# Optimization experiments

Hardware: AMD Instinct MI355X
Metric: run time of the kernel (lower is better)

Reference implementation:

```python
import jax, jax.numpy as jnp
import numpy as np

N_NODES = 4096
N_EDGES = 16384
L = 512
MP_STEPS = 5
DT = 0.01


def _mlp(x, W1, b1, W2, b2):
    return jax.nn.relu(x @ W1 + b1) @ W2 + b2


def _ln(x):
    m = jnp.mean(x, axis=-1, keepdims=True)
    v = jnp.var(x, axis=-1, keepdims=True)
    return (x - m) * jax.lax.rsqrt(v + 1e-6)


_PARAM_SHAPES = [
    ("enc_e_W1", (1, L)), ("enc_e_b1", (L,)), ("enc_e_W2", (L, L)), ("enc_e_b2", (L,)),
    ("enc_n_W1", (1, L)), ("enc_n_b1", (L,)), ("enc_n_W2", (L, L)), ("enc_n_b2", (L,)),
    ("proc_e_W1", (3 * L, L)), ("proc_e_b1", (L,)), ("proc_e_W2", (L, L)), ("proc_e_b2", (L,)),
    ("proc_n_W1", (2 * L, L)), ("proc_n_b1", (L,)), ("proc_n_W2", (L, L)), ("proc_n_b2", (L,)),
    ("dec_e_W1", (L, L)), ("dec_e_b1", (L,)), ("dec_e_W2", (L, 1)), ("dec_e_b2", (1,)),
]


def setup_inputs() -> dict:
    key = jax.random.key(0)
    ks = jax.random.split(key, 3 + len(_PARAM_SHAPES))
    d = {}
    d["state"] = jax.random.normal(ks[0], (N_EDGES + N_NODES,), dtype=jnp.float32)
    d["senders"] = jax.random.randint(ks[1], (N_EDGES,), 0, N_NODES)
    d["receivers"] = jax.random.randint(ks[2], (N_EDGES,), 0, N_NODES)
    for i, (name, shp) in enumerate(_PARAM_SHAPES):
        if name.endswith(("b1", "b2")):
            d[name] = jnp.zeros(shp, dtype=jnp.float32)
        else:
            d[name] = 0.02 * jax.random.normal(ks[3 + i], shp, dtype=jnp.float32)
    return d


def _hamiltonian(x, senders, receivers,
                 enc_e_W1, enc_e_b1, enc_e_W2, enc_e_b2,
                 enc_n_W1, enc_n_b1, enc_n_W2, enc_n_b2,
                 proc_e_W1, proc_e_b1, proc_e_W2, proc_e_b2,
                 proc_n_W1, proc_n_b1, proc_n_W2, proc_n_b2,
                 dec_e_W1, dec_e_b1, dec_e_W2, dec_e_b2):
    # graph_from_state: edge scalars then node scalars
    e = x[:N_EDGES].reshape(N_EDGES, 1)
    n = x[N_EDGES:].reshape(N_NODES, 1)
    # encode (MLP + layer norm)
    eh = _ln(_mlp(e, enc_e_W1, enc_e_b1, enc_e_W2, enc_e_b2))  # [E, L]
    nh = _ln(_mlp(n, enc_n_W1, enc_n_b1, enc_n_W2, enc_n_b2))  # [N, L]
    # process: num_mp_steps of GraphNetwork-style message passing, shared params
    for _ in range(MP_STEPS):
        msg_in = jnp.concatenate([eh, nh[senders], nh[receivers]], axis=-1)  # [E, 3L]
        eh = eh + _mlp(msg_in, proc_e_W1, proc_e_b1, proc_e_W2, proc_e_b2)
        agg = jax.ops.segment_sum(eh, receivers, num_segments=N_NODES)  # [N, L]
        node_in = jnp.concatenate([nh, agg], axis=-1)  # [N, 2L]
        nh = nh + _mlp(node_in, proc_n_W1, proc_n_b1, proc_n_W2, proc_n_b2)
    # decode edges to scalars; H = sum of decoded edge energies
    dec_e = _mlp(eh, dec_e_W1, dec_e_b1, dec_e_W2, dec_e_b2)  # [E, 1]
    return jnp.sum(dec_e)


def reference(state, senders, receivers,
              enc_e_W1, enc_e_b1, enc_e_W2, enc_e_b2,
              enc_n_W1, enc_n_b1, enc_n_W2, enc_n_b2,
              proc_e_W1, proc_e_b1, proc_e_W2, proc_e_b2,
              proc_n_W1, proc_n_b1, proc_n_W2, proc_n_b2,
              dec_e_W1, dec_e_b1, dec_e_W2, dec_e_b2):
    def H_fn(x):
        return _hamiltonian(x, senders, receivers,
                            enc_e_W1, enc_e_b1, enc_e_W2, enc_e_b2,
                            enc_n_W1, enc_n_b1, enc_n_W2, enc_n_b2,
                            proc_e_W1, proc_e_b1, proc_e_W2, proc_e_b2,
                            proc_n_W1, proc_n_b1, proc_n_W2, proc_n_b2,
                            dec_e_W1, dec_e_b1, dec_e_W2, dec_e_b2)
    H, dH = jax.value_and_grad(H_fn)(state)
    # one integrator step driven by the Hamiltonian gradient (stand-in for DAE solve)
    next_state = state - DT * dH
    return next_state
```

## Files before the change

### kernel.cpp

```cpp
#include <hip/hip_runtime.h>


#define E_ROWS 16384
#define N_ROWS 4096
#define DT_F   0.01f

typedef unsigned char u8;
typedef unsigned short u16;
typedef __attribute__((ext_vector_type(8))) short short8v;
typedef __attribute__((ext_vector_type(4))) float f32x4;

__device__ __forceinline__ u16 f2b(float f) {
    union { float f; unsigned u; } v; v.f = f;
    unsigned r = v.u + 0x7FFF + ((v.u >> 16) & 1);
    return (u16)(r >> 16);
}
__device__ __forceinline__ float b2f(u16 u) {
    union { unsigned u; float f; } v; v.u = ((unsigned)u) << 16;
    return v.f;
}

template<int BM, int WM, int WN, int KTOT, int LDA, int LDC,
         bool ADD_C, bool GATHER2, bool BIAS, bool RELU_MASK, bool APPLY_MASK,
         bool WF32, bool WBF16, bool DUALOUT, bool ROWDOT, bool DECW2>
__global__ __launch_bounds__(256)
void bgemm(const u16* __restrict__ A, const u16* __restrict__ Bt,
           float* __restrict__ C, u16* __restrict__ Cb,
           const u16* __restrict__ Cinb, const float* __restrict__ bias,
           const u16* __restrict__ G12b,
           const int* __restrict__ sidx, const int* __restrict__ ridx,
           u8* __restrict__ maskw, u16* __restrict__ C2b,
           const float* __restrict__ wvec, float* __restrict__ outp)
{
    constexpr int BN = WN * 64;
    constexpr int NA = BM / 16;
    constexpr int TC = (BM + BN) / 16;
    constexpr int PER = TC / 4;
    constexpr int IFRAG = BM / WM / 16;
    __shared__ u16 Ls[TC * 512];

    const int tid = threadIdx.x;
    const int lane = tid & 63;
    const int wv = tid >> 6;
    const int wr = wv / WN;
    const int wc = wv % WN;

    const int gx = gridDim.x;
    int id = blockIdx.y * gx + blockIdx.x;
    const int nwg = gx * gridDim.y;
    id = (id & 7) * (nwg >> 3) + (id >> 3);
    const int bx = id % gx;
    const int by = id / gx;
    const int rowBase = by * BM;
    const int colBase = bx * BN;

    const int srow = lane & 15;
    const int slotk = (lane >> 4) << 3;

    const u16* srcs[PER];
    u16* dsts[PER];
#pragma unroll
    for (int q = 0; q < PER; ++q) {
        const int c = wv + (q << 2);
        if (c < NA)
            srcs[q] = A + (size_t)(rowBase + c * 16 + srow) * LDA + slotk;
        else
            srcs[q] = Bt + (size_t)(colBase + (c - NA) * 16 + srow) * KTOT + slotk;
        dsts[q] = Ls + c * 512;
    }

    f32x4 acc[IFRAG][4];
#pragma unroll
    for (int i = 0; i < IFRAG; ++i)
#pragma unroll
        for (int j = 0; j < 4; ++j)
            acc[i][j] = (f32x4){0.f, 0.f, 0.f, 0.f};

    const int fro = ((lane >> 4) << 7) + ((lane & 15) << 3);

    for (int kb = 0; kb < KTOT; kb += 32) {
#pragma unroll
        for (int q = 0; q < PER; ++q)
            __builtin_amdgcn_global_load_lds(
                (const __attribute__((address_space(1))) void*)(srcs[q] + kb),
                (__attribute__((address_space(3))) void*)dsts[q], 16, 0, 0);
        __syncthreads();
        short8v af[IFRAG], bfm[4];
#pragma unroll
        for (int i = 0; i < IFRAG; ++i)
            af[i] = *(const short8v*)&Ls[((wr * IFRAG + i) << 9) + fro];
#pragma unroll
        for (int j = 0; j < 4; ++j)
            bfm[j] = *(const short8v*)&Ls[((NA + (wc << 2) + j) << 9) + fro];
#pragma unroll
        for (int i = 0; i < IFRAG; ++i)
#pragma unroll
            for (int j = 0; j < 4; ++j)
                acc[i][j] = __builtin_amdgcn_mfma_f32_16x16x32_bf16(af[i], bfm[j], acc[i][j], 0, 0, 0);
        __syncthreads();
    }

    const int colB = colBase + wc * 64 + (lane & 15);
    const int rowB = rowBase + wr * (BM / WM) + ((lane >> 4) << 2);
    float bcol[4], wv4[4];
    if (BIAS) {
#pragma unroll
        for (int j = 0; j < 4; ++j) bcol[j] = bias[colB + (j << 4)];
    }
    if (ROWDOT || DECW2) {
#pragma unroll
        for (int j = 0; j < 4; ++j) wv4[j] = wvec[colB + (j << 4)];
    }
    const bool upper = DUALOUT && (colBase >= 512);
#pragma unroll
    for (int i = 0; i < IFRAG; ++i) {
#pragma unroll
        for (int r = 0; r < 4; ++r) {
            const int row = rowB + (i << 4) + r;
            int si = 0, ri = 0;
            if (GATHER2) { si = sidx[row]; ri = ridx[row]; }
            float rds = 0.f;
#pragma unroll
            for (int j = 0; j < 4; ++j) {
                const int col = colB + (j << 4);
                float v = acc[i][j][r];
                if (DUALOUT && upper) {
                    C2b[(size_t)row * 512 + (col - 512)] = f2b(v);
                    continue;
                }
                if (GATHER2) v += b2f(G12b[(size_t)si * 1024 + col]) + b2f(G12b[(size_t)ri * 1024 + 512 + col]);
                if (ADD_C) v += b2f(Cinb[(size_t)row * LDC + col]);
                if (BIAS) v += bcol[j];
                if (DECW2) {
                    Cb[(size_t)row * LDC + col] = (v > 0.f) ? f2b(wv4[j]) : (u16)0;
                    continue;
                }
                if (RELU_MASK) {
                    const u8 m = v > 0.f;
                    maskw[(size_t)row * 512 + col] = m;
                    v = m ? v : 0.f;
                }
                if (APPLY_MASK) {
                    if (!maskw[(size_t)row * 512 + col]) v = 0.f;
                }
                if (ROWDOT) rds += v * wv4[j];
                const size_t o = (size_t)row * LDC + col;
                if (WF32) C[o] = v;
                if (WBF16) Cb[o] = f2b(v);
            }
            if (ROWDOT) {
#pragma unroll
                for (int m = 1; m < 16; m <<= 1) rds += __shfl_xor(rds, m);
                if ((lane & 15) == 0) atomicAdd(outp + row, -DT_F * rds);
            }
        }
    }
}

struct WArgs {
    const float* src[10];
    u16* dstP[10];
    u16* dstT[10];
    int ldP[10], ldT[10];
};

__global__ void wcvt_kernel(WArgs a)
{
    const int i = blockIdx.z;
    const float* W = a.src[i];
    u16* P = a.dstP[i]; const int lp = a.ldP[i];
    u16* T = a.dstT[i]; const int lt = a.ldT[i];
    __shared__ u16 t[64][66];
    const int rb = blockIdx.y << 6, cb = blockIdx.x << 6;
    const int tr = threadIdx.x >> 4;
    const int tc = (threadIdx.x & 15) << 2;
#pragma unroll
    for (int rr = 0; rr < 4; ++rr) {
        const int r = tr + (rr << 4);
        const float4 v = *(const float4*)&W[(size_t)(rb + r) * 512 + cb + tc];
        ushort4 u; u.x = f2b(v.x); u.y = f2b(v.y); u.z = f2b(v.z); u.w = f2b(v.w);
        *(ushort4*)&P[(size_t)(rb + r) * lp + cb + tc] = u;
        t[r][tc] = u.x; t[r][tc + 1] = u.y; t[r][tc + 2] = u.z; t[r][tc + 3] = u.w;
    }
    __syncthreads();
#pragma unroll
    for (int rr = 0; rr < 4; ++rr) {
        const int n = tr + (rr << 4);
        ushort4 u;
        u.x = t[tc][n]; u.y = t[tc + 1][n]; u.z = t[tc + 2][n]; u.w = t[tc + 3][n];
        *(ushort4*)&T[(size_t)(cb + n) * lt + rb + tc] = u;
    }
}

__device__ void csr_build(const int* __restrict__ idx, int* __restrict__ starts,
                          int* __restrict__ eids)
{
    __shared__ int hist[4096];
    __shared__ int scanbuf[1024];
    const int t = threadIdx.x;
    for (int i = t; i < 4096; i += 1024) hist[i] = 0;
    __syncthreads();
    for (int e = t; e < 16384; e += 1024) atomicAdd(&hist[idx[e]], 1);
    __syncthreads();
    const int base = t << 2;
    const int l0 = hist[base], l1 = hist[base + 1], l2 = hist[base + 2], l3 = hist[base + 3];
    const int lsum = l0 + l1 + l2 + l3;
    scanbuf[t] = lsum;
    __syncthreads();
    for (int ofs = 1; ofs < 1024; ofs <<= 1) {
        const int v = scanbuf[t];
        const int u = (t >= ofs) ? scanbuf[t - ofs] : 0;
        __syncthreads();
        scanbuf[t] = v + u;
        __syncthreads();
    }
    const int excl = scanbuf[t] - lsum;
    const int p0 = excl, p1 = p0 + l0, p2 = p1 + l1, p3 = p2 + l2;
    starts[base] = p0; starts[base + 1] = p1; starts[base + 2] = p2; starts[base + 3] = p3;
    if (t == 0) starts[4096] = 16384;
    __syncthreads();
    hist[base] = p0; hist[base + 1] = p1; hist[base + 2] = p2; hist[base + 3] = p3;
    __syncthreads();
    for (int e = t; e < 16384; e += 1024) {
        const int pos = atomicAdd(&hist[idx[e]], 1);
        eids[pos] = e;
    }
    __syncthreads();
    for (int n = t; n < 4096; n += 1024) {
        const int s0 = starts[n], s1 = hist[n];
        for (int i = s0 + 1; i < s1; ++i) {
            const int v = eids[i];
            int j = i - 1;
            while (j >= s0 && eids[j] > v) { eids[j + 1] = eids[j]; --j; }
            eids[j + 1] = v;
        }
    }
}

__global__ __launch_bounds__(1024) void csr2_kernel(const int* __restrict__ senders,
                                                    const int* __restrict__ receivers,
                                                    int* __restrict__ sst, int* __restrict__ seid,
                                                    int* __restrict__ rst, int* __restrict__ reid)
{
    if (blockIdx.x == 0) csr_build(receivers, rst, reid);
    else                 csr_build(senders, sst, seid);
}

__global__ void init_out_kernel(const float* __restrict__ state, float* __restrict__ out)
{
    const int t = blockIdx.x * 256 + threadIdx.x;
    out[t] = state[t];
}

__global__ void seg_agg_fwd_kernel(const u16* __restrict__ ehb, const int* __restrict__ starts,
                                   const int* __restrict__ eids, const u16* __restrict__ nhb,
                                   u16* __restrict__ nagg)
{
    const int n = blockIdx.x, c = threadIdx.x;
    const int s0 = starts[n], s1 = starts[n + 1];
    float a0 = 0.f, a1 = 0.f;
    for (int i = s0; i < s1; ++i) {
        const u16* p = ehb + (size_t)eids[i] * 512;
        a0 += b2f(p[c]); a1 += b2f(p[c + 256]);
    }
    u16* d = nagg + (size_t)n * 1024;
    const u16* s = nhb + (size_t)n * 512;
    d[c] = s[c]; d[c + 256] = s[c + 256];
    d[512 + c] = f2b(a0); d[768 + c] = f2b(a1);
}

__global__ void seg_sr_bwd_kernel(const u16* __restrict__ dh1e,
                                  const int* __restrict__ sst, const int* __restrict__ seid,
                                  const int* __restrict__ rst, const int* __restrict__ reid,
                                  u16* __restrict__ SR)
{
    const int n = blockIdx.x, c = threadIdx.x;
    float a0 = 0.f, a1 = 0.f, b0 = 0.f, b1 = 0.f;
    for (int i = sst[n]; i < sst[n + 1]; ++i) {
        const u16* p = dh1e + (size_t)seid[i] * 512;
        a0 += b2f(p[c]); a1 += b2f(p[c + 256]);
    }
    for (int i = rst[n]; i < rst[n + 1]; ++i) {
        const u16* p = dh1e + (size_t)reid[i] * 512;
        b0 += b2f(p[c]); b1 += b2f(p[c + 256]);
    }
    u16* d = SR + (size_t)n * 1024;
    d[c] = f2b(a0); d[c + 256] = f2b(a1);
    d[512 + c] = f2b(b0); d[768 + c] = f2b(b1);
}

__global__ void enc_h1_kernel(const float* __restrict__ x, const float* __restrict__ W1,
                              const float* __restrict__ b1, u16* __restrict__ h1b,
                              u8* __restrict__ mask)
{
    const int idx = blockIdx.x * 256 + threadIdx.x;
    const int row = idx >> 7;
    const int c = (idx & 127) << 2;
    const float xv = x[row];
    const float4 w = *(const float4*)&W1[c];
    const float4 b = *(const float4*)&b1[c];
    float4 v;
    v.x = fmaf(xv, w.x, b.x); v.y = fmaf(xv, w.y, b.y);
    v.z = fmaf(xv, w.z, b.z); v.w = fmaf(xv, w.w, b.w);
    uchar4 m;
    m.x = v.x > 0.f; m.y = v.y > 0.f; m.z = v.z > 0.f; m.w = v.w > 0.f;
    v.x = m.x ? v.x : 0.f; v.y = m.y ? v.y : 0.f;
    v.z = m.z ? v.z : 0.f; v.w = m.w ? v.w : 0.f;
    const size_t o = (size_t)row * 512 + c;
    ushort4 u; u.x = f2b(v.x); u.y = f2b(v.y); u.z = f2b(v.z); u.w = f2b(v.w);
    *(ushort4*)&h1b[o] = u;
    *(uchar4*)&mask[o] = m;
}

__global__ void ln_fwd_kernel(const float* __restrict__ x, u16* __restrict__ xhat_b,
                              u16* __restrict__ xb, float* __restrict__ rstd_save)
{
    const int row = blockIdx.x, tid = threadIdx.x;
    const float* p = x + (size_t)row * 512;
    const float a = p[tid], b = p[tid + 256];
    __shared__ float s1[256], s2[256];
    s1[tid] = a + b; s2[tid] = a * a + b * b;
    __syncthreads();
    for (int d = 128; d > 0; d >>= 1) {
        if (tid < d) { s1[tid] += s1[tid + d]; s2[tid] += s2[tid + d]; }
        __syncthreads();
    }
    const float mean = s1[0] * (1.f / 512.f);
    const float var = s2[0] * (1.f / 512.f) - mean * mean;
    const float r = rsqrtf(var + 1e-6f);
    const float ya = (a - mean) * r, yb = (b - mean) * r;
    const size_t o = (size_t)row * 512 + tid;
    xhat_b[o] = f2b(ya); xhat_b[o + 256] = f2b(yb);
    xb[o] = f2b(ya); xb[o + 256] = f2b(yb);
    if (tid == 0) rstd_save[row] = r;
}

__global__ void ln_bwd_kernel(u16* __restrict__ d, const u16* __restrict__ xhat_b,
                              const float* __restrict__ rstd)
{
    const int row = blockIdx.x, tid = threadIdx.x;
    u16* p = d + (size_t)row * 512;
    const u16* xh = xhat_b + (size_t)row * 512;
    const float da = b2f(p[tid]), dbv = b2f(p[tid + 256]);
    const float xa = b2f(xh[tid]), xbv = b2f(xh[tid + 256]);
    __shared__ float s1[256], s2[256];
    s1[tid] = da + dbv; s2[tid] = da * xa + dbv * xbv;
    __syncthreads();
    for (int dd = 128; dd > 0; dd >>= 1) {
        if (tid < dd) { s1[tid] += s1[tid + dd]; s2[tid] += s2[tid + dd]; }
        __syncthreads();
    }
    const float m1 = s1[0] * (1.f / 512.f);
    const float m2 = s2[0] * (1.f / 512.f);
    const float r = rstd[row];
    p[tid] = f2b(r * (da - m1 - xa * m2));
    p[tid + 256] = f2b(r * (dbv - m1 - xbv * m2));
}

__global__ void gather_add_kernel(u16* __restrict__ dst, const u16* __restrict__ src,
                                  const int* __restrict__ idx)
{
    const int t = blockIdx.x * 256 + threadIdx.x;
    const int row = t >> 6;
    const int c = (t & 63) << 3;
    const size_t o = (size_t)row * 512 + c;
    short8v a = *(const short8v*)&dst[o];
    const short8v g = *(const short8v*)&src[(size_t)idx[row] * 512 + c];
    short8v r;
#pragma unroll
    for (int i = 0; i < 8; ++i)
        r[i] = (short)f2b(b2f((u16)a[i]) + b2f((u16)g[i]));
    *(short8v*)&dst[o] = r;
}

extern "C" void kernel_launch(void* const* d_in, const int* in_sizes, int n_in,
                              void* d_out, int out_size, void* d_ws, size_t ws_size,
                              hipStream_t stream)
{
    (void)in_sizes; (void)n_in; (void)out_size; (void)ws_size;
    const float* state     = (const float*)d_in[0];
    const int*   senders   = (const int*)d_in[1];
    const int*   receivers = (const int*)d_in[2];
    const float* enc_e_W1 = (const float*)d_in[3];
    const float* enc_e_b1 = (const float*)d_in[4];
    const float* enc_e_W2 = (const float*)d_in[5];
    const float* enc_e_b2 = (const float*)d_in[6];
    const float* enc_n_W1 = (const float*)d_in[7];
    const float* enc_n_b1 = (const float*)d_in[8];
    const float* enc_n_W2 = (const float*)d_in[9];
    const float* enc_n_b2 = (const float*)d_in[10];
    const float* pe_W1 = (const float*)d_in[11];
    const float* pe_b1 = (const float*)d_in[12];
    const float* pe_W2 = (const float*)d_in[13];
    const float* pe_b2 = (const float*)d_in[14];
    const float* pn_W1 = (const float*)d_in[15];
    const float* pn_b1 = (const float*)d_in[16];
    const float* pn_W2 = (const float*)d_in[17];
    const float* pn_b2 = (const float*)d_in[18];
    const float* de_W1 = (const float*)d_in[19];
    const float* de_b1 = (const float*)d_in[20];
    const float* de_W2 = (const float*)d_in[21];
    float* out = (float*)d_out;

    const size_t EL = (size_t)E_ROWS * 512, NL = (size_t)N_ROWS * 512;
    const size_t LL = 512 * 512;
    char* w = (char*)d_ws;
    size_t off = 0;
    auto carve = [&](size_t bytes) -> char* {
        char* p = w + off;
        off += (bytes + 255) & ~(size_t)255;
        return p;
    };
    u16* wb = (u16*)carve(20 * LL * 2);
    u16* WT0 = wb;           u16* WT1 = wb + LL;      u16* WT2 = wb + 2 * LL;
    u16* WT34 = wb + 3 * LL;                          u16* WT5 = wb + 5 * LL;
    u16* WT8 = wb + 6 * LL;  u16* WT9 = wb + 7 * LL;
    u16* WP0 = wb + 8 * LL;  u16* WP1 = wb + 9 * LL;  u16* WP2 = wb + 10 * LL;
    u16* WP5 = wb + 11 * LL; u16* WP8 = wb + 12 * LL; u16* WP9 = wb + 13 * LL;
    u16* WT67 = wb + 14 * LL;
    u16* WP34c = wb + 16 * LL;
    u16* WP67 = wb + 18 * LL;

    float* eh  = (float*)carve(EL * 4);
    float* nh  = (float*)carve(NL * 4);
    u16* G1b   = (u16*)carve(NL * 2);
    u16* G12b  = (u16*)carve(NL * 2 * 2);
    u16* nsr   = (u16*)carve(NL * 2 * 2);
    u16* eh0b = (u16*)carve(EL * 2);
    u16* nh0b = (u16*)carve(NL * 2);
    u16* ehb  = (u16*)carve(EL * 2);
    u16* h1eb = (u16*)carve(EL * 2);
    u16* nhb  = (u16*)carve(NL * 2);
    u16* h1nb = (u16*)carve(NL * 2);
    float* rstd_e = (float*)carve(E_ROWS * 4);
    float* rstd_n = (float*)carve(N_ROWS * 4);
    u8* menc_e = (u8*)carve(EL);
    u8* menc_n = (u8*)carve(NL);
    u8* mpe    = (u8*)carve(5 * EL);
    u8* mpn    = (u8*)carve(5 * NL);
    int* rst  = (int*)carve(4097 * 4);
    int* reid = (int*)carve(16384 * 4);
    int* sst  = (int*)carve(4097 * 4);
    int* seid = (int*)carve(16384 * 4);

    const dim3 blk(256);
    const dim3 gE(4, E_ROWS / 128);
    const dim3 gN(4, N_ROWS / 64);
    const dim3 gN1024(8, N_ROWS / 64);
    const float* fp = nullptr;
    u16* up = nullptr;
    const u16* cup = nullptr;
    const int* ip = nullptr;
    u8* mp = nullptr;
    float* f2p = nullptr;

    WArgs wa;
    const float* wsrc[10] = { enc_e_W2, enc_n_W2, pe_W1, pe_W1 + LL, pe_W1 + 2 * LL,
                              pe_W2, pn_W1, pn_W1 + LL, pn_W2, de_W1 };
    u16* dstP[10] = { WP0, WP1, WP2, WP34c, WP34c + 512, WP5, WP67, WP67 + LL, WP8, WP9 };
    int  ldP [10] = { 512, 512, 512, 1024,  1024,        512, 512,  512,       512, 512 };
    u16* dstT[10] = { WT0, WT1, WT2, WT34, WT34 + LL, WT5, WT67, WT67 + 512, WT8, WT9 };
    int  ldT [10] = { 512, 512, 512, 512,  512,       512, 1024, 1024,       512, 512 };
    for (int i = 0; i < 10; ++i) {
        wa.src[i] = wsrc[i]; wa.dstP[i] = dstP[i]; wa.dstT[i] = dstT[i];
        wa.ldP[i] = ldP[i]; wa.ldT[i] = ldT[i];
    }
    wcvt_kernel<<<dim3(8, 8, 10), blk, 0, stream>>>(wa);

    csr2_kernel<<<2, 1024, 0, stream>>>(senders, receivers, sst, seid, rst, reid);
    init_out_kernel<<<(E_ROWS + N_ROWS) / 256, blk, 0, stream>>>(state, out);

    enc_h1_kernel<<<E_ROWS * 128 / 256, blk, 0, stream>>>(state, enc_e_W1, enc_e_b1, h1eb, menc_e);
    bgemm<128,2,2,512,512,512, false,false,true,false,false, true,false,false,false,false>
        <<<gE, blk, 0, stream>>>(h1eb, WT0, eh, up, cup, enc_e_b2, cup, ip, ip, mp, up, fp, f2p);
    ln_fwd_kernel<<<E_ROWS, blk, 0, stream>>>(eh, eh0b, ehb, rstd_e);
    enc_h1_kernel<<<N_ROWS * 128 / 256, blk, 0, stream>>>(state + E_ROWS, enc_n_W1, enc_n_b1, h1nb, menc_n);
    bgemm<64,2,2,512,512,512, false,false,true,false,false, true,false,false,false,false>
        <<<gN, blk, 0, stream>>>(h1nb, WT1, nh, up, cup, enc_n_b2, cup, ip, ip, mp, up, fp, f2p);
    ln_fwd_kernel<<<N_ROWS, blk, 0, stream>>>(nh, nh0b, nhb, rstd_n);

    for (int k = 0; k < 5; ++k) {
        bgemm<64,2,2,512,512,1024, false,false,false,false,false, false,true,false,false,false>
            <<<gN1024, blk, 0, stream>>>(nhb, WT34, f2p, G12b, cup, fp, cup, ip, ip, mp, up, fp, f2p);
        bgemm<128,2,2,512,512,512, false,true,true,true,false, false,true,false,false,false>
            <<<gE, blk, 0, stream>>>(ehb, WT2, f2p, h1eb, cup, pe_b1, G12b, senders, receivers, mpe + (size_t)k * EL, up, fp, f2p);
        bgemm<128,2,2,512,512,512, true,false,true,false,false, false,true,false,false,false>
            <<<gE, blk, 0, stream>>>(h1eb, WT5, f2p, ehb, ehb, pe_b2, cup, ip, ip, mp, up, fp, f2p);
        seg_agg_fwd_kernel<<<N_ROWS, blk, 0, stream>>>(ehb, rst, reid, nhb, nsr);
        bgemm<64,2,2,1024,1024,512, false,false,true,true,false, false,true,false,false,false>
            <<<gN, blk, 0, stream>>>(nsr, WT67, f2p, h1nb, cup, pn_b1, cup, ip, ip, mpn + (size_t)k * NL, up, fp, f2p);
        bgemm<64,2,2,512,512,512, true,false,true,false,false, false,true,false,false,false>
            <<<gN, blk, 0, stream>>>(h1nb, WT8, f2p, nhb, nhb, pn_b2, cup, ip, ip, mp, up, fp, f2p);
    }

    bgemm<128,2,2,512,512,512, false,false,true,false,false, false,false,false,false,true>
        <<<gE, blk, 0, stream>>>(ehb, WT9, f2p, h1eb, cup, de_b1, cup, ip, ip, mp, up, de_W2, f2p);

    bgemm<128,2,2,512,512,512, false,false,false,false,false, false,true,false,false,false>
        <<<gE, blk, 0, stream>>>(h1eb, WP9, f2p, ehb, cup, fp, cup, ip, ip, mp, up, fp, f2p);

    for (int k = 4; k >= 0; --k) {
        if (k < 4) {
            bgemm<64,2,2,512,512,512, false,false,false,false,true, false,true,false,false,false>
                <<<gN, blk, 0, stream>>>(nhb, WP8, f2p, h1nb, cup, fp, cup, ip, ip, mpn + (size_t)k * NL, up, fp, f2p);
            bgemm<64,2,2,512,512,512, true,false,false,false,false, false,true,true,false,false>
                <<<gN1024, blk, 0, stream>>>(h1nb, WP67, f2p, nhb, nhb, fp, cup, ip, ip, mp, G1b, fp, f2p);
            gather_add_kernel<<<E_ROWS * 64 / 256, blk, 0, stream>>>(ehb, G1b, receivers);
        }
        bgemm<128,2,2,512,512,512, false,false,false,false,true, false,true,false,false,false>
            <<<gE, blk, 0, stream>>>(ehb, WP5, f2p, h1eb, cup, fp, cup, ip, ip, mpe + (size_t)k * EL, up, fp, f2p);
        bgemm<128,2,2,512,512,512, true,false,false,false,false, false,true,false,false,false>
            <<<gE, blk, 0, stream>>>(h1eb, WP2, f2p, ehb, ehb, fp, cup, ip, ip, mp, up, fp, f2p);
        seg_sr_bwd_kernel<<<N_ROWS, blk, 0, stream>>>(h1eb, sst, seid, rst, reid, nsr);
        if (k == 4)
            bgemm<64,2,2,1024,1024,512, false,false,false,false,false, false,true,false,false,false>
                <<<gN, blk, 0, stream>>>(nsr, WP34c, f2p, nhb, cup, fp, cup, ip, ip, mp, up, fp, f2p);
        else
            bgemm<64,2,2,1024,1024,512, true,false,false,false,false, false,true,false,false,false>
                <<<gN, blk, 0, stream>>>(nsr, WP34c, f2p, nhb, nhb, fp, cup, ip, ip, mp, up, fp, f2p);
    }

    ln_bwd_kernel<<<E_ROWS, blk, 0, stream>>>(ehb, eh0b, rstd_e);
    bgemm<128,2,2,512,512,512, false,false,false,false,true, false,false,false,true,false>
        <<<gE, blk, 0, stream>>>(ehb, WP0, f2p, up, cup, fp, cup, ip, ip, menc_e, up, enc_e_W1, out);
    ln_bwd_kernel<<<N_ROWS, blk, 0, stream>>>(nhb, nh0b, rstd_n);
    bgemm<64,2,2,512,512,512, false,false,false,false,true, false,false,false,true,false>
        <<<gN, blk, 0, stream>>>(nhb, WP1, f2p, up, cup, fp, cup, ip, ip, menc_n, up, enc_n_W1, out + E_ROWS);
}
```

Before: 1.359 ms.

## Double-buffer GEMM LDS tiles, merge edge/node encoder passes, retile node GEMMs

The bf16 MFMA GEMM now uses two LDS buffers, so the next K-tile's global-to-LDS load is issued while the current tile is consumed, and one barrier per K step is dropped. The edge and node encoder and final backward stages are merged into single launches over a contiguous 20480-row buffer, with a BSEL flag that picks the weights, bias and wvec per row block. Node-side GEMMs switch to a 4x1 warp layout with 64-wide N tiles, which doubles their grid size. Costs are twice the LDS per block, which may lower occupancy, and the edge and node buffers must now sit contiguously in the workspace.

```diff
diff --git a/kernel.cpp b/kernel.cpp
--- a/kernel.cpp
+++ b/kernel.cpp
@@ -3,6 +3,7 @@
 
 #define E_ROWS 16384
 #define N_ROWS 4096
+#define ALL_ROWS 20480
 #define DT_F   0.01f
 
 typedef unsigned char u8;
@@ -22,22 +23,24 @@
 
 template<int BM, int WM, int WN, int KTOT, int LDA, int LDC,
          bool ADD_C, bool GATHER2, bool BIAS, bool RELU_MASK, bool APPLY_MASK,
-         bool WF32, bool WBF16, bool DUALOUT, bool ROWDOT, bool DECW2>
+         bool WF32, bool WBF16, bool DUALOUT, bool ROWDOT, bool DECW2, bool BSEL>
 __global__ __launch_bounds__(256)
-void bgemm(const u16* __restrict__ A, const u16* __restrict__ Bt,
+void bgemm(const u16* __restrict__ A, const u16* __restrict__ Bt, const u16* __restrict__ Bt2,
            float* __restrict__ C, u16* __restrict__ Cb,
            const u16* __restrict__ Cinb, const float* __restrict__ bias,
-           const u16* __restrict__ G12b,
+           const float* __restrict__ bias2, const u16* __restrict__ G12b,
            const int* __restrict__ sidx, const int* __restrict__ ridx,
            u8* __restrict__ maskw, u16* __restrict__ C2b,
-           const float* __restrict__ wvec, float* __restrict__ outp)
+           const float* __restrict__ wvec, const float* __restrict__ wvec2,
+           float* __restrict__ outp)
 {
     constexpr int BN = WN * 64;
     constexpr int NA = BM / 16;
     constexpr int TC = (BM + BN) / 16;
     constexpr int PER = TC / 4;
+    constexpr int NT = KTOT / 32;
     constexpr int IFRAG = BM / WM / 16;
-    __shared__ u16 Ls[TC * 512];
+    __shared__ u16 Ls[2][TC * 512];
 
     const int tid = threadIdx.x;
     const int lane = tid & 63;
@@ -54,19 +57,24 @@
     const int rowBase = by * BM;
     const int colBase = bx * BN;
 
+    const u16* BtU = Bt;
+    const float* biasU = bias;
+    const float* wvecU = wvec;
+    if (BSEL && rowBase >= E_ROWS) { BtU = Bt2; biasU = bias2; wvecU = wvec2; }
+
     const int srow = lane & 15;
     const int slotk = (lane >> 4) << 3;
 
     const u16* srcs[PER];
-    u16* dsts[PER];
+    int dstoff[PER];
 #pragma unroll
     for (int q = 0; q < PER; ++q) {
         const int c = wv + (q << 2);
         if (c < NA)
             srcs[q] = A + (size_t)(rowBase + c * 16 + srow) * LDA + slotk;
         else
-            srcs[q] = Bt + (size_t)(colBase + (c - NA) * 16 + srow) * KTOT + slotk;
-        dsts[q] = Ls + c * 512;
+            srcs[q] = BtU + (size_t)(colBase + (c - NA) * 16 + srow) * KTOT + slotk;
+        dstoff[q] = c * 512;
     }
 
     f32x4 acc[IFRAG][4];
@@ -78,26 +86,42 @@
 
     const int fro = ((lane >> 4) << 7) + ((lane & 15) << 3);
 
-    for (int kb = 0; kb < KTOT; kb += 32) {
-#pragma unroll
-        for (int q = 0; q < PER; ++q)
-            __builtin_amdgcn_global_load_lds(
-                (const __attribute__((address_space(1))) void*)(srcs[q] + kb),
-                (__attribute__((address_space(3))) void*)dsts[q], 16, 0, 0);
-        __syncthreads();
+#pragma unroll
+    for (int q = 0; q < PER; ++q)
+        __builtin_amdgcn_global_load_lds(
+            (const __attribute__((address_space(1))) void*)srcs[q],
+            (__attribute__((address_space(3))) void*)&Ls[0][dstoff[q]], 16, 0, 0);
+    asm volatile("s_waitcnt vmcnt(0)" ::: "memory");
+    __builtin_amdgcn_s_barrier();
+    asm volatile("" ::: "memory");
+
+#pragma unroll
+    for (int t = 0; t < NT; ++t) {
+        const int cur = t & 1;
+        if (t + 1 < NT) {
+#pragma unroll
+            for (int q = 0; q < PER; ++q)
+                __builtin_amdgcn_global_load_lds(
+                    (const __attribute__((address_space(1))) void*)(srcs[q] + (t + 1) * 32),
+                    (__attribute__((address_space(3))) void*)&Ls[cur ^ 1][dstoff[q]], 16, 0, 0);
+        }
         short8v af[IFRAG], bfm[4];
 #pragma unroll
         for (int i = 0; i < IFRAG; ++i)
-            af[i] = *(const short8v*)&Ls[((wr * IFRAG + i) << 9) + fro];
+            af[i] = *(const short8v*)&Ls[cur][((wr * IFRAG + i) << 9) + fro];
 #pragma unroll
         for (int j = 0; j < 4; ++j)
-            bfm[j] = *(const short8v*)&Ls[((NA + (wc << 2) + j) << 9) + fro];
+            bfm[j] = *(const short8v*)&Ls[cur][((NA + (wc << 2) + j) << 9) + fro];
 #pragma unroll
         for (int i = 0; i < IFRAG; ++i)
 #pragma unroll
             for (int j = 0; j < 4; ++j)
                 acc[i][j] = __builtin_amdgcn_mfma_f32_16x16x32_bf16(af[i], bfm[j], acc[i][j], 0, 0, 0);
-        __syncthreads();
+        if (t + 1 < NT) {
+            asm volatile("s_waitcnt vmcnt(0)" ::: "memory");
+            __builtin_amdgcn_s_barrier();
+            asm volatile("" ::: "memory");
+        }
     }
 
     const int colB = colBase + wc * 64 + (lane & 15);
@@ -105,11 +129,11 @@
     float bcol[4], wv4[4];
     if (BIAS) {
 #pragma unroll
-        for (int j = 0; j < 4; ++j) bcol[j] = bias[colB + (j << 4)];
+        for (int j = 0; j < 4; ++j) bcol[j] = biasU[colB + (j << 4)];
     }
     if (ROWDOT || DECW2) {
 #pragma unroll
-        for (int j = 0; j < 4; ++j) wv4[j] = wvec[colB + (j << 4)];
+        for (int j = 0; j < 4; ++j) wv4[j] = wvecU[colB + (j << 4)];
     }
     const bool upper = DUALOUT && (colBase >= 512);
 #pragma unroll
@@ -289,13 +313,17 @@
     d[512 + c] = f2b(b0); d[768 + c] = f2b(b1);
 }
 
-__global__ void enc_h1_kernel(const float* __restrict__ x, const float* __restrict__ W1,
-                              const float* __restrict__ b1, u16* __restrict__ h1b,
-                              u8* __restrict__ mask)
+__global__ void enc_h1_kernel(const float* __restrict__ x,
+                              const float* __restrict__ W1e, const float* __restrict__ b1e,
+                              const float* __restrict__ W1n, const float* __restrict__ b1n,
+                              u16* __restrict__ h1b, u8* __restrict__ mask)
 {
     const int idx = blockIdx.x * 256 + threadIdx.x;
     const int row = idx >> 7;
     const int c = (idx & 127) << 2;
+    const bool edge = row < E_ROWS;
+    const float* W1 = edge ? W1e : W1n;
+    const float* b1 = edge ? b1e : b1n;
     const float xv = x[row];
     const float4 w = *(const float4*)&W1[c];
     const float4 b = *(const float4*)&b1[c];
@@ -403,6 +431,7 @@
     float* out = (float*)d_out;
 
     const size_t EL = (size_t)E_ROWS * 512, NL = (size_t)N_ROWS * 512;
+    const size_t AL = (size_t)ALL_ROWS * 512;
     const size_t LL = 512 * 512;
     char* w = (char*)d_ws;
     size_t off = 0;
@@ -421,21 +450,18 @@
     u16* WP34c = wb + 16 * LL;
     u16* WP67 = wb + 18 * LL;
 
-    float* eh  = (float*)carve(EL * 4);
-    float* nh  = (float*)carve(NL * 4);
+    float* eh  = (float*)carve(AL * 4);
+    u16* ehb   = (u16*)carve(EL * 2);
+    u16* nhb   = (u16*)carve(NL * 2);
+    u16* h1eb  = (u16*)carve(EL * 2);
+    u16* h1nb  = (u16*)carve(NL * 2);
+    u16* eh0b  = (u16*)carve(EL * 2);
+    u16* nh0b  = (u16*)carve(NL * 2);
+    u8* menc   = (u8*)carve(AL);
     u16* G1b   = (u16*)carve(NL * 2);
     u16* G12b  = (u16*)carve(NL * 2 * 2);
     u16* nsr   = (u16*)carve(NL * 2 * 2);
-    u16* eh0b = (u16*)carve(EL * 2);
-    u16* nh0b = (u16*)carve(NL * 2);
-    u16* ehb  = (u16*)carve(EL * 2);
-    u16* h1eb = (u16*)carve(EL * 2);
-    u16* nhb  = (u16*)carve(NL * 2);
-    u16* h1nb = (u16*)carve(NL * 2);
-    float* rstd_e = (float*)carve(E_ROWS * 4);
-    float* rstd_n = (float*)carve(N_ROWS * 4);
-    u8* menc_e = (u8*)carve(EL);
-    u8* menc_n = (u8*)carve(NL);
+    float* rstd = (float*)carve(ALL_ROWS * 4);
     u8* mpe    = (u8*)carve(5 * EL);
     u8* mpn    = (u8*)carve(5 * NL);
     int* rst  = (int*)carve(4097 * 4);
@@ -445,8 +471,9 @@
 
     const dim3 blk(256);
     const dim3 gE(4, E_ROWS / 128);
-    const dim3 gN(4, N_ROWS / 64);
-    const dim3 gN1024(8, N_ROWS / 64);
+    const dim3 gA(4, ALL_ROWS / 128);
+    const dim3 gN512(8, N_ROWS / 64);
+    const dim3 gN1024(16, N_ROWS / 64);
     const float* fp = nullptr;
     u16* up = nullptr;
     const u16* cup = nullptr;
@@ -468,62 +495,56 @@
     wcvt_kernel<<<dim3(8, 8, 10), blk, 0, stream>>>(wa);
 
     csr2_kernel<<<2, 1024, 0, stream>>>(senders, receivers, sst, seid, rst, reid);
-    init_out_kernel<<<(E_ROWS + N_ROWS) / 256, blk, 0, stream>>>(state, out);
-
-    enc_h1_kernel<<<E_ROWS * 128 / 256, blk, 0, stream>>>(state, enc_e_W1, enc_e_b1, h1eb, menc_e);
-    bgemm<128,2,2,512,512,512, false,false,true,false,false, true,false,false,false,false>
-        <<<gE, blk, 0, stream>>>(h1eb, WT0, eh, up, cup, enc_e_b2, cup, ip, ip, mp, up, fp, f2p);
-    ln_fwd_kernel<<<E_ROWS, blk, 0, stream>>>(eh, eh0b, ehb, rstd_e);
-    enc_h1_kernel<<<N_ROWS * 128 / 256, blk, 0, stream>>>(state + E_ROWS, enc_n_W1, enc_n_b1, h1nb, menc_n);
-    bgemm<64,2,2,512,512,512, false,false,true,false,false, true,false,false,false,false>
-        <<<gN, blk, 0, stream>>>(h1nb, WT1, nh, up, cup, enc_n_b2, cup, ip, ip, mp, up, fp, f2p);
-    ln_fwd_kernel<<<N_ROWS, blk, 0, stream>>>(nh, nh0b, nhb, rstd_n);
+    init_out_kernel<<<ALL_ROWS / 256, blk, 0, stream>>>(state, out);
+
+    enc_h1_kernel<<<ALL_ROWS * 128 / 256, blk, 0, stream>>>(state, enc_e_W1, enc_e_b1,
+                                                            enc_n_W1, enc_n_b1, h1eb, menc);
+    bgemm<128,2,2,512,512,512, false,false,true,false,false, true,false,false,false,false,true>
+        <<<gA, blk, 0, stream>>>(h1eb, WT0, WT1, eh, up, cup, enc_e_b2, enc_n_b2, cup, ip, ip, mp, up, fp, fp, f2p);
+    ln_fwd_kernel<<<ALL_ROWS, blk, 0, stream>>>(eh, eh0b, ehb, rstd);
 
     for (int k = 0; k < 5; ++k) {
-        bgemm<64,2,2,512,512,1024, false,false,false,false,false, false,true,false,false,false>
-            <<<gN1024, blk, 0, stream>>>(nhb, WT34, f2p, G12b, cup, fp, cup, ip, ip, mp, up, fp, f2p);
-        bgemm<128,2,2,512,512,512, false,true,true,true,false, false,true,false,false,false>
-            <<<gE, blk, 0, stream>>>(ehb, WT2, f2p, h1eb, cup, pe_b1, G12b, senders, receivers, mpe + (size_t)k * EL, up, fp, f2p);
-        bgemm<128,2,2,512,512,512, true,false,true,false,false, false,true,false,false,false>
-            <<<gE, blk, 0, stream>>>(h1eb, WT5, f2p, ehb, ehb, pe_b2, cup, ip, ip, mp, up, fp, f2p);
+        bgemm<64,4,1,512,512,1024, false,false,false,false,false, false,true,false,false,false,false>
+            <<<gN1024, blk, 0, stream>>>(nhb, WT34, cup, f2p, G12b, cup, fp, fp, cup, ip, ip, mp, up, fp, fp, f2p);
+        bgemm<128,2,2,512,512,512, false,true,true,true,false, false,true,false,false,false,false>
+            <<<gE, blk, 0, stream>>>(ehb, WT2, cup, f2p, h1eb, cup, pe_b1, fp, G12b, senders, receivers, mpe + (size_t)k * EL, up, fp, fp, f2p);
+        bgemm<128,2,2,512,512,512, true,false,true,false,false, false,true,false,false,false,false>
+            <<<gE, blk, 0, stream>>>(h1eb, WT5, cup, f2p, ehb, ehb, pe_b2, fp, cup, ip, ip, mp, up, fp, fp, f2p);
         seg_agg_fwd_kernel<<<N_ROWS, blk, 0, stream>>>(ehb, rst, reid, nhb, nsr);
-        bgemm<64,2,2,1024,1024,512, false,false,true,true,false, false,true,false,false,false>
-            <<<gN, blk, 0, stream>>>(nsr, WT67, f2p, h1nb, cup, pn_b1, cup, ip, ip, mpn + (size_t)k * NL, up, fp, f2p);
-        bgemm<64,2,2,512,512,512, true,false,true,false,false, false,true,false,false,false>
-            <<<gN, blk, 0, stream>>>(h1nb, WT8, f2p, nhb, nhb, pn_b2, cup, ip, ip, mp, up, fp, f2p);
-    }
-
-    bgemm<128,2,2,512,512,512, false,false,true,false,false, false,false,false,false,true>
-        <<<gE, blk, 0, stream>>>(ehb, WT9, f2p, h1eb, cup, de_b1, cup, ip, ip, mp, up, de_W2, f2p);
-
-    bgemm<128,2,2,512,512,512, false,false,false,false,false, false,true,false,false,false>
-        <<<gE, blk, 0, stream>>>(h1eb, WP9, f2p, ehb, cup, fp, cup, ip, ip, mp, up, fp, f2p);
+        bgemm<64,4,1,1024,1024,512, false,false,true,true,false, false,true,false,false,false,false>
+            <<<gN512, blk, 0, stream>>>(nsr, WT67, cup, f2p, h1nb, cup, pn_b1, fp, cup, ip, ip, mpn + (size_t)k * NL, up, fp, fp, f2p);
+        bgemm<64,4,1,512,512,512, true,false,true,false,false, false,true,false,false,false,false>
+            <<<gN512, blk, 0, stream>>>(h1nb, WT8, cup, f2p, nhb, nhb, pn_b2, fp, cup, ip, ip, mp, up, fp, fp, f2p);
+    }
+
+    bgemm<128,2,2,512,512,512, false,false,true,false,false, false,false,false,false,true,false>
+        <<<gE, blk, 0, stream>>>(ehb, WT9, cup, f2p, h1eb, cup, de_b1, fp, cup, ip, ip, mp, up, de_W2, fp, f2p);
+
+    bgemm<128,2,2,512,512,512, false,false,false,false,false, false,true,false,false,false,false>
+        <<<gE, blk, 0, stream>>>(h1eb, WP9, cup, f2p, ehb, cup, fp, fp, cup, ip, ip, mp, up, fp, fp, f2p);
 
     for (int k = 4; k >= 0; --k) {
         if (k < 4) {
-            bgemm<64,2,2,512,512,512, false,false,false,false,true, false,true,false,false,false>
-                <<<gN, blk, 0, stream>>>(nhb, WP8, f2p, h1nb, cup, fp, cup, ip, ip, mpn + (size_t)k * NL, up, fp, f2p);
-            bgemm<64,2,2,512,512,512, true,false,false,false,false, false,true,true,false,false>
-                <<<gN1024, blk, 0, stream>>>(h1nb, WP67, f2p, nhb, nhb, fp, cup, ip, ip, mp, G1b, fp, f2p);
+            bgemm<64,4,1,512,512,512, false,false,false,false,true, false,true,false,false,false,false>
+                <<<gN512, blk, 0, stream>>>(nhb, WP8, cup, f2p, h1nb, cup, fp, fp, cup, ip, ip, mpn + (size_t)k * NL, up, fp, fp, f2p);
+            bgemm<64,4,1,512,512,512, true,false,false,false,false, false,true,true,false,false,false>
+                <<<gN1024, blk, 0, stream>>>(h1nb, WP67, cup, f2p, nhb, nhb, fp, fp, cup, ip, ip, mp, G1b, fp, fp, f2p);
             gather_add_kernel<<<E_ROWS * 64 / 256, blk, 0, stream>>>(ehb, G1b, receivers);
         }
-        bgemm<128,2,2,512,512,512, false,false,false,false,true, false,true,false,false,false>
-            <<<gE, blk, 0, stream>>>(ehb, WP5, f2p, h1eb, cup, fp, cup, ip, ip, mpe + (size_t)k * EL, up, fp, f2p);
-        bgemm<128,2,2,512,512,512, true,false,false,false,false, false,true,false,false,false>
-            <<<gE, blk, 0, stream>>>(h1eb, WP2, f2p, ehb, ehb, fp, cup, ip, ip, mp, up, fp, f2p);
+        bgemm<128,2,2,512,512,512, false,false,false,false,true, false,true,false,false,false,false>
+            <<<gE, blk, 0, stream>>>(ehb, WP5, cup, f2p, h1eb, cup, fp, fp, cup, ip, ip, mpe + (size_t)k * EL, up, fp, fp, f2p);
+        bgemm<128,2,2,512,512,512, true,false,false,false,false, false,true,false,false,false,false>
+            <<<gE, blk, 0, stream>>>(h1eb, WP2, cup, f2p, ehb, ehb, fp, fp, cup, ip, ip, mp, up, fp, fp, f2p);
         seg_sr_bwd_kernel<<<N_ROWS, blk, 0, stream>>>(h1eb, sst, seid, rst, reid, nsr);
         if (k == 4)
-            bgemm<64,2,2,1024,1024,512, false,false,false,false,false, false,true,false,false,false>
-                <<<gN, blk, 0, stream>>>(nsr, WP34c, f2p, nhb, cup, fp, cup, ip, ip, mp, up, fp, f2p);
+            bgemm<64,4,1,1024,1024,512, false,false,false,false,false, false,true,false,false,false,false>
+                <<<gN512, blk, 0, stream>>>(nsr, WP34c, cup, f2p, nhb, cup, fp, fp, cup, ip, ip, mp, up, fp, fp, f2p);
         else
-            bgemm<64,2,2,1024,1024,512, true,false,false,false,false, false,true,false,false,false>
-                <<<gN, blk, 0, stream>>>(nsr, WP34c, f2p, nhb, nhb, fp, cup, ip, ip, mp, up, fp, f2p);
-    }
-
-    ln_bwd_kernel<<<E_ROWS, blk, 0, stream>>>(ehb, eh0b, rstd_e);
-    bgemm<128,2,2,512,512,512, false,false,false,false,true, false,false,false,true,false>
-        <<<gE, blk, 0, stream>>>(ehb, WP0, f2p, up, cup, fp, cup, ip, ip, menc_e, up, enc_e_W1, out);
-    ln_bwd_kernel<<<N_ROWS, blk, 0, stream>>>(nhb, nh0b, rstd_n);
-    bgemm<64,2,2,512,512,512, false,false,false,false,true, false,false,false,true,false>
-        <<<gN, blk, 0, stream>>>(nhb, WP1, f2p, up, cup, fp, cup, ip, ip, menc_n, up, enc_n_W1, out + E_ROWS);
-}
+            bgemm<64,4,1,1024,1024,512, true,false,false,false,false, false,true,false,false,false,false>
+                <<<gN512, blk, 0, stream>>>(nsr, WP34c, cup, f2p, nhb, nhb, fp, fp, cup, ip, ip, mp, up, fp, fp, f2p);
+    }
+
+    ln_bwd_kernel<<<ALL_ROWS, blk, 0, stream>>>(ehb, eh0b, rstd);
+    bgemm<128,2,2,512,512,512, false,false,false,false,true, false,false,false,true,false,true>
+        <<<gA, blk, 0, stream>>>(ehb, WP0, WP1, f2p, up, cup, fp, fp, cup, ip, ip, menc, up, enc_e_W1, enc_n_W1, out);
+}
```

After: 1.390 ms. 1.02x slower.
